# Optimization experiments

Measured on AMD Instinct MI355X. Metric: run time of the kernel, lower is better.

## Reference

```python
import jax, jax.numpy as jnp
import numpy as np

B = 2097152   # number of material points (2**21)
NS = [32, 32] # ICNN hidden widths; output layer is Dense(1)


def setup_inputs() -> dict:
    key = jax.random.key(0)
    ks = jax.random.split(key, 7)
    # Deformation gradients near identity so C = F^T F is invertible.
    F = jnp.eye(3, dtype=jnp.float32)[None, :, :] + 0.05 * jax.random.normal(
        ks[0], (B, 3, 3), dtype=jnp.float32)
    dims = [6] + NS + [1]
    inp = {"F": F}
    for i in range(3):
        # non_neg kernel constraint -> positive weights
        inp[f"W{i}"] = 0.5 * jax.random.uniform(ks[1 + 2 * i], (dims[i], dims[i + 1]),
                                                dtype=jnp.float32)
        inp[f"b{i}"] = 0.1 * jax.random.normal(ks[2 + 2 * i], (dims[i + 1],),
                                               dtype=jnp.float32)
    return inp


def _energy(F, W0, b0, W1, b1, W2, b2):
    """Invariants layer + ICNN -> scalar potential W per sample, shape [B,1]."""
    # C = F^T F, batched 3x3
    C = jnp.einsum('bji,bjk->bik', F, F)
    J = jnp.linalg.det(F)                          # [B]
    cof_C = jnp.linalg.det(C)[:, None, None] * jnp.linalg.inv(C)  # [B,3,3]
    tr = lambda A: jnp.trace(A, axis1=-2, axis2=-1)
    dg = lambda A: jnp.diagonal(A, axis1=-2, axis2=-1)
    I_1 = tr(C)
    I_2 = tr(cof_C)
    # NOTE: TF code uses trace(C ** 2) with ELEMENTWISE square -> sum of squared diagonal
    I_7 = jnp.sum(dg(C) ** 2, axis=-1)
    I_11 = jnp.sum(dg(cof_C) ** 2, axis=-1)
    i = jnp.stack([I_1, I_2, J, -J, I_7, I_11], axis=1)  # [B,6]
    h = jax.nn.softplus(i @ W0 + b0)
    h = jax.nn.softplus(h @ W1 + b1)
    return h @ W2 + b2                              # [B,1]


def reference(F, W0, b0, W1, b1, W2, b2):
    # GradientTape: P = dW/dF (per-sample, since samples are independent)
    Wv, vjp_fn = jax.vjp(lambda f: _energy(f, W0, b0, W1, b1, W2, b2), F)
    P, = vjp_fn(jnp.ones_like(Wv))
    return (P, Wv)
```

## Files before the change

### kernel.cpp

```cpp
#include <hip/hip_runtime.h>
#include <math.h>

typedef __attribute__((ext_vector_type(8)))  short  bf16x8;
typedef __attribute__((ext_vector_type(16))) float  f32x16;

union FragU { unsigned u[4]; bf16x8 s; };

__device__ __forceinline__ float fast_rcp(float x) { return __builtin_amdgcn_rcpf(x); }

__device__ __forceinline__ unsigned cvtpk(float lo, float hi) {
    unsigned r;
    asm("v_cvt_pk_bf16_f32 %0, %1, %2" : "=v"(r) : "v"(lo), "v"(hi));
    return r;
}
__device__ __forceinline__ unsigned pswapu(unsigned x) { return (unsigned)__shfl_xor((int)x, 32, 64); }
__device__ __forceinline__ float    pswapf(float x)    { return __shfl_xor(x, 32, 64); }
__device__ __forceinline__ float bfl(unsigned p) { return __uint_as_float(p << 16); }
__device__ __forceinline__ float bfh(unsigned p) { return __uint_as_float(p & 0xffff0000u); }

__device__ __forceinline__ void sp_sig(float z, float& h, float& s) {
    float az = fabsf(z);
    float e  = __expf(-az);
    float r  = fast_rcp(1.0f + e);
    h = fmaxf(z, 0.0f) + __logf(1.0f + e);
    s = (z >= 0.0f) ? r : (1.0f - r);
}

__device__ __forceinline__ FragU bfrag(bool low, unsigned a0, unsigned a1, unsigned a2, unsigned a3) {
    unsigned s0 = pswapu(a0), s1 = pswapu(a1), s2 = pswapu(a2), s3 = pswapu(a3);
    FragU f;
    f.u[0] = low ? a0 : s2;
    f.u[1] = low ? a1 : s3;
    f.u[2] = low ? s0 : a2;
    f.u[3] = low ? s1 : a3;
    return f;
}

__global__ __launch_bounds__(256) void energy_kernel(
    const float* __restrict__ Fg,
    const float* __restrict__ W0, const float* __restrict__ b0,
    const float* __restrict__ W1, const float* __restrict__ b1,
    const float* __restrict__ W2, const float* __restrict__ b2,
    float* __restrict__ P, float* __restrict__ Wv, int n)
{
    const int  tid  = threadIdx.x;
    const int  lane = tid & 63;
    const int  wid  = tid >> 6;
    const int  col  = lane & 31;
    const int  half = lane >> 5;
    const bool low  = (half == 0);
    const long wave_base = ((long)blockIdx.x * 4 + wid) * 64;
    const long idx  = wave_base + lane;
    const long cidx = (idx < n) ? idx : 0;

    FragU w0t, w1t[2], w1f[2], w0b[2];
    #pragma unroll
    for (int p = 0; p < 4; ++p) {
        const int k0 = half*8 + 2*p, k1 = k0 + 1;
        float lo = (k0 < 6) ? W0[k0*32 + col] : ((k0 == 6) ? b0[col] : 0.f);
        float hi = (k1 < 6) ? W0[k1*32 + col] : ((k1 == 6) ? b0[col] : 0.f);
        w0t.u[p] = cvtpk(lo, hi);
    }
    #pragma unroll
    for (int hf = 0; hf < 2; ++hf) {
        #pragma unroll
        for (int p = 0; p < 4; ++p) {
            const int k0 = hf*16 + half*8 + 2*p, k1 = k0 + 1;
            w1t[hf].u[p] = cvtpk(W1[k0*32 + col], W1[k1*32 + col]);
            w1f[hf].u[p] = cvtpk(W1[col*32 + k0], W1[col*32 + k1]);
            float lo = (col < 6) ? W0[col*32 + k0] : 0.f;
            float hi = (col < 6) ? W0[col*32 + k1] : 0.f;
            w0b[hf].u[p] = cvtpk(lo, hi);
        }
    }
    unsigned b1p[8], w2p[8];
    #pragma unroll
    for (int p = 0; p < 8; ++p) {
        const int r0 = 2*p, r1 = r0 + 1;
        const int R0 = (r0 & 3) + 8*(r0 >> 2) + 4*half;
        const int R1 = (r1 & 3) + 8*(r1 >> 2) + 4*half;
        b1p[p] = cvtpk(b1[R0], b1[R1]);
        w2p[p] = cvtpk(W2[R0], W2[R1]);
    }
    const float b2v = b2[0];

    const float* fp = Fg + cidx * 9;
    float iv0, iv1, iv2, iv4, iv5;
    {
        float f00=fp[0], f01=fp[1], f02=fp[2];
        float f10=fp[3], f11=fp[4], f12=fp[5];
        float f20=fp[6], f21=fp[7], f22=fp[8];

        float c00 = f00*f00 + f10*f10 + f20*f20;
        float c01 = f00*f01 + f10*f11 + f20*f21;
        float c02 = f00*f02 + f10*f12 + f20*f22;
        float c11 = f01*f01 + f11*f11 + f21*f21;
        float c12 = f01*f02 + f11*f12 + f21*f22;
        float c22 = f02*f02 + f12*f12 + f22*f22;

        float A00 = c11*c22 - c12*c12;
        float A01 = c02*c12 - c01*c22;
        float A02 = c01*c12 - c02*c11;
        float A11 = c00*c22 - c02*c02;
        float A12 = c01*c02 - c00*c12;
        float A22 = c00*c11 - c01*c01;

        iv0 = c00 + c11 + c22;
        iv1 = A00 + A11 + A22;
        iv2 = f00*(f11*f22 - f12*f21) - f01*(f10*f22 - f12*f20) + f02*(f10*f21 - f11*f20);
        iv4 = c00*c00 + c11*c11 + c22*c22;
        iv5 = A00*A00 + A11*A11 + A22*A22;
    }

    unsigned V01 = cvtpk(iv0, iv1);
    unsigned V23 = cvtpk(iv2, -iv2);
    unsigned V45 = cvtpk(iv4, iv5);
    const unsigned C67 = cvtpk(1.0f, 0.0f);

    float pt_[2];
    float dk[2][4];

    #pragma unroll
    for (int t = 0; t < 2; ++t) {
        FragU biv;
        if (t == 0) { biv.u[0]=V01;        biv.u[1]=V23;        biv.u[2]=V45;        biv.u[3]=C67; }
        else        { biv.u[0]=pswapu(V01); biv.u[1]=pswapu(V23); biv.u[2]=pswapu(V45); biv.u[3]=C67; }

        f32x16 zz;
        #pragma unroll
        for (int r = 0; r < 16; ++r) zz[r] = 0.f;

        f32x16 z0 = __builtin_amdgcn_mfma_f32_32x32x16_bf16(w0t.s, biv.s, zz, 0, 0, 0);

        unsigned hpk[8], s0p[8];
        #pragma unroll
        for (int p = 0; p < 8; ++p) {
            float ha, sa, hb, sb;
            sp_sig(z0[2*p],   ha, sa);
            sp_sig(z0[2*p+1], hb, sb);
            hpk[p] = cvtpk(ha, hb);
            s0p[p] = cvtpk(sa, sb);
        }
        FragU hb0 = bfrag(low, hpk[0], hpk[1], hpk[2], hpk[3]);
        FragU hb1 = bfrag(low, hpk[4], hpk[5], hpk[6], hpk[7]);

        f32x16 z1;
        #pragma unroll
        for (int p = 0; p < 8; ++p) { z1[2*p] = bfl(b1p[p]); z1[2*p+1] = bfh(b1p[p]); }
        z1 = __builtin_amdgcn_mfma_f32_32x32x16_bf16(w1t[0].s, hb0.s, z1, 0, 0, 0);
        z1 = __builtin_amdgcn_mfma_f32_32x32x16_bf16(w1t[1].s, hb1.s, z1, 0, 0, 0);

        float pt = 0.f;
        unsigned gpk[8];
        #pragma unroll
        for (int p = 0; p < 8; ++p) {
            float h1a, s1a, h1b, s1b;
            sp_sig(z1[2*p],   h1a, s1a);
            sp_sig(z1[2*p+1], h1b, s1b);
            float wa = bfl(w2p[p]), wb = bfh(w2p[p]);
            pt = fmaf(h1a, wa, pt);
            pt = fmaf(h1b, wb, pt);
            gpk[p] = cvtpk(wa * s1a, wb * s1b);
        }
        pt_[t] = pt;
        FragU gb0 = bfrag(low, gpk[0], gpk[1], gpk[2], gpk[3]);
        FragU gb1 = bfrag(low, gpk[4], gpk[5], gpk[6], gpk[7]);

        #pragma unroll
        for (int r = 0; r < 16; ++r) zz[r] = 0.f;
        f32x16 gh = __builtin_amdgcn_mfma_f32_32x32x16_bf16(w1f[0].s, gb0.s, zz, 0, 0, 0);
        gh = __builtin_amdgcn_mfma_f32_32x32x16_bf16(w1f[1].s, gb1.s, gh, 0, 0, 0);

        unsigned qpk[8];
        #pragma unroll
        for (int p = 0; p < 8; ++p)
            qpk[p] = cvtpk(gh[2*p] * bfl(s0p[p]), gh[2*p+1] * bfh(s0p[p]));
        FragU qb0 = bfrag(low, qpk[0], qpk[1], qpk[2], qpk[3]);
        FragU qb1 = bfrag(low, qpk[4], qpk[5], qpk[6], qpk[7]);

        #pragma unroll
        for (int r = 0; r < 16; ++r) zz[r] = 0.f;
        f32x16 da = __builtin_amdgcn_mfma_f32_32x32x16_bf16(w0b[0].s, qb0.s, zz, 0, 0, 0);
        da = __builtin_amdgcn_mfma_f32_32x32x16_bf16(w0b[1].s, qb1.s, da, 0, 0, 0);
        dk[t][0] = da[0]; dk[t][1] = da[1]; dk[t][2] = da[2]; dk[t][3] = da[3];
    }

    float po0 = pswapf(pt_[0]);
    float po1 = pswapf(pt_[1]);
    float wvv = (low ? (pt_[0] + po0) : (pt_[1] + po1)) + b2v;

    float s10 = pswapf(dk[1][0]), s11 = pswapf(dk[1][1]);
    float s12 = pswapf(dk[1][2]), s13 = pswapf(dk[1][3]);
    float s00 = pswapf(dk[0][0]), s01 = pswapf(dk[0][1]);
    float d0  = low ? dk[0][0] : s10;
    float d1  = low ? dk[0][1] : s11;
    float d2r = low ? dk[0][2] : s12;
    float d3r = low ? dk[0][3] : s13;
    float d4  = low ? s00 : dk[1][0];
    float d5  = low ? s01 : dk[1][1];

    float f00=fp[0], f01=fp[1], f02=fp[2];
    float f10=fp[3], f11=fp[4], f12=fp[5];
    float f20=fp[6], f21=fp[7], f22=fp[8];

    float c00 = f00*f00 + f10*f10 + f20*f20;
    float c01 = f00*f01 + f10*f11 + f20*f21;
    float c02 = f00*f02 + f10*f12 + f20*f22;
    float c11 = f01*f01 + f11*f11 + f21*f21;
    float c12 = f01*f02 + f11*f12 + f21*f22;
    float c22 = f02*f02 + f12*f12 + f22*f22;

    float A00 = c11*c22 - c12*c12;
    float A01 = c02*c12 - c01*c22;
    float A02 = c01*c12 - c02*c11;
    float A11 = c00*c22 - c02*c02;
    float A12 = c01*c02 - c00*c12;
    float A22 = c00*c11 - c01*c01;

    float cf00 = f11*f22 - f12*f21;
    float cf01 = f12*f20 - f10*f22;
    float cf02 = f10*f21 - f11*f20;
    float cf10 = f02*f21 - f01*f22;
    float cf11 = f00*f22 - f02*f20;
    float cf12 = f01*f20 - f00*f21;
    float cf20 = f01*f12 - f02*f11;
    float cf21 = f02*f10 - f00*f12;
    float cf22 = f00*f11 - f01*f10;
    float J  = f00*cf00 + f01*cf01 + f02*cf02;
    float I1 = c00 + c11 + c22;
    float I11v = A00*A00 + A11*A11 + A22*A22;

    float inv2 = 2.0f * fast_rcp(J * J);

    float T00 = A00*A00*A00 + A11*A01*A01 + A22*A02*A02;
    float T01 = A00*A00*A01 + A11*A01*A11 + A22*A02*A12;
    float T02 = A00*A00*A02 + A11*A01*A12 + A22*A02*A22;
    float T11 = A00*A01*A01 + A11*A11*A11 + A22*A12*A12;
    float T12 = A00*A01*A02 + A11*A11*A12 + A22*A12*A22;
    float T22 = A00*A02*A02 + A11*A12*A12 + A22*A22*A22;

    float G00 = inv2 * (I11v*A00 - T00);
    float G01 = inv2 * (I11v*A01 - T01);
    float G02 = inv2 * (I11v*A02 - T02);
    float G11e= inv2 * (I11v*A11 - T11);
    float G12 = inv2 * (I11v*A12 - T12);
    float G22 = inv2 * (I11v*A22 - T22);

    float aJ  = d2r - d3r;
    float t1  = 2.0f * d0;
    float t2  = 2.0f * d1;
    float t7  = 4.0f * d4;
    float t11 = 2.0f * d5;

    float m00 = t1 + t2*(I1 - c00) + t7*c00 + t11*G00;
    float m01 =      -t2*c01               + t11*G01;
    float m02 =      -t2*c02               + t11*G02;
    float m11 = t1 + t2*(I1 - c11) + t7*c11 + t11*G11e;
    float m12 =      -t2*c12               + t11*G12;
    float m22 = t1 + t2*(I1 - c22) + t7*c22 + t11*G22;

    if (idx < n) {
        float* p = P + idx * 9;
        p[0] = f00*m00 + f01*m01 + f02*m02 + aJ*cf00;
        p[1] = f00*m01 + f01*m11 + f02*m12 + aJ*cf01;
        p[2] = f00*m02 + f01*m12 + f02*m22 + aJ*cf02;
        p[3] = f10*m00 + f11*m01 + f12*m02 + aJ*cf10;
        p[4] = f10*m01 + f11*m11 + f12*m12 + aJ*cf11;
        p[5] = f10*m02 + f11*m12 + f12*m22 + aJ*cf12;
        p[6] = f20*m00 + f21*m01 + f22*m02 + aJ*cf20;
        p[7] = f20*m01 + f21*m11 + f22*m12 + aJ*cf21;
        p[8] = f20*m02 + f21*m12 + f22*m22 + aJ*cf22;
        Wv[idx] = wvv;
    }
}

extern "C" void kernel_launch(void* const* d_in, const int* in_sizes, int n_in,
                              void* d_out, int out_size, void* d_ws, size_t ws_size,
                              hipStream_t stream) {
    const float* F  = (const float*)d_in[0];
    const float* W0 = (const float*)d_in[1];
    const float* b0 = (const float*)d_in[2];
    const float* W1 = (const float*)d_in[3];
    const float* b1 = (const float*)d_in[4];
    const float* W2 = (const float*)d_in[5];
    const float* b2 = (const float*)d_in[6];
    int n = in_sizes[0] / 9;
    float* out = (float*)d_out;
    float* P  = out;
    float* Wv = out + (size_t)n * 9;

    int block = 256;
    int grid = (n + block - 1) / block;
    hipLaunchKernelGGL(energy_kernel, dim3(grid), dim3(block), 0, stream,
                       F, W0, b0, W1, b1, W2, b2, P, Wv, n);
}
```

Baseline: 135.9 us.

## Prepack MFMA weight fragments and permute K to drop cross-half shuffles

Adds a one-wave pre-kernel that converts the weights to bf16 and stores them in per-lane MFMA fragment order in workspace. The main kernel then fetches them with a few vector loads instead of many scattered scalar loads and conversions per thread. The K index of the W1/W0-back fragments is permuted (rho) so MFMA output registers can feed the next MFMA's B operand directly, which removes the bfrag lane-swap shuffles between layers. This costs an extra kernel launch and a dependency on workspace, and correctness rests on the permutation matching the accumulator layout.

```diff
diff --git a/kernel.cpp b/kernel.cpp
--- a/kernel.cpp
+++ b/kernel.cpp
@@ -4,7 +4,7 @@
 typedef __attribute__((ext_vector_type(8)))  short  bf16x8;
 typedef __attribute__((ext_vector_type(16))) float  f32x16;
 
-union FragU { unsigned u[4]; bf16x8 s; };
+union FragU { unsigned u[4]; bf16x8 s; uint4 q; };
 
 __device__ __forceinline__ float fast_rcp(float x) { return __builtin_amdgcn_rcpf(x); }
 
@@ -17,6 +17,11 @@
 __device__ __forceinline__ float    pswapf(float x)    { return __shfl_xor(x, 32, 64); }
 __device__ __forceinline__ float bfl(unsigned p) { return __uint_as_float(p << 16); }
 __device__ __forceinline__ float bfh(unsigned p) { return __uint_as_float(p & 0xffff0000u); }
+
+__device__ __forceinline__ int rho(int s) {
+    int f = s >> 4, h = (s >> 3) & 1, p = (s >> 1) & 3, j = s & 1;
+    return 16*f + 4*h + 8*(p >> 1) + 2*(p & 1) + j;
+}
 
 __device__ __forceinline__ void sp_sig(float z, float& h, float& s) {
     float az = fabsf(z);
@@ -26,63 +31,86 @@
     s = (z >= 0.0f) ? r : (1.0f - r);
 }
 
-__device__ __forceinline__ FragU bfrag(bool low, unsigned a0, unsigned a1, unsigned a2, unsigned a3) {
-    unsigned s0 = pswapu(a0), s1 = pswapu(a1), s2 = pswapu(a2), s3 = pswapu(a3);
-    FragU f;
-    f.u[0] = low ? a0 : s2;
-    f.u[1] = low ? a1 : s3;
-    f.u[2] = low ? s0 : a2;
-    f.u[3] = low ? s1 : a3;
-    return f;
-}
-
-__global__ __launch_bounds__(256) void energy_kernel(
-    const float* __restrict__ Fg,
+__global__ __launch_bounds__(64) void pack_weights(
     const float* __restrict__ W0, const float* __restrict__ b0,
     const float* __restrict__ W1, const float* __restrict__ b1,
     const float* __restrict__ W2, const float* __restrict__ b2,
+    unsigned* __restrict__ ws)
+{
+    const int lane = threadIdx.x;
+    const int col = lane & 31, half = lane >> 5;
+
+    unsigned v[4];
+    #pragma unroll
+    for (int p = 0; p < 4; ++p) {
+        const int k0 = half*8 + 2*p, k1 = k0 + 1;
+        float lo = (k0 < 6) ? W0[k0*32 + col] : ((k0 == 6) ? b0[col] : 0.f);
+        float hi = (k1 < 6) ? W0[k1*32 + col] : ((k1 == 6) ? b0[col] : 0.f);
+        v[p] = cvtpk(lo, hi);
+    }
+    *(uint4*)(ws + lane*4) = make_uint4(v[0], v[1], v[2], v[3]);
+
+    #pragma unroll
+    for (int hf = 0; hf < 2; ++hf) {
+        unsigned t[4], fq[4], bq[4];
+        #pragma unroll
+        for (int p = 0; p < 4; ++p) {
+            const int s0 = hf*16 + half*8 + 2*p;
+            const int r0 = rho(s0), r1 = r0 + 1;
+            t[p]  = cvtpk(W1[r0*32 + col], W1[r1*32 + col]);
+            fq[p] = cvtpk(W1[col*32 + r0], W1[col*32 + r1]);
+            float lo = (col < 6) ? W0[col*32 + r0] : 0.f;
+            float hi = (col < 6) ? W0[col*32 + r1] : 0.f;
+            bq[p] = cvtpk(lo, hi);
+        }
+        *(uint4*)(ws + 256  + lane*8 + hf*4) = make_uint4(t[0],  t[1],  t[2],  t[3]);
+        *(uint4*)(ws + 768  + lane*8 + hf*4) = make_uint4(fq[0], fq[1], fq[2], fq[3]);
+        *(uint4*)(ws + 1280 + lane*8 + hf*4) = make_uint4(bq[0], bq[1], bq[2], bq[3]);
+    }
+
+    unsigned bp[8], wp[8];
+    #pragma unroll
+    for (int p = 0; p < 8; ++p) {
+        const int r0 = 2*p, r1 = r0 + 1;
+        const int R0 = (r0 & 3) + 8*(r0 >> 2) + 4*half;
+        const int R1 = (r1 & 3) + 8*(r1 >> 2) + 4*half;
+        bp[p] = cvtpk(b1[R0], b1[R1]);
+        wp[p] = cvtpk(W2[R0], W2[R1]);
+    }
+    *(uint4*)(ws + 1792 + lane*8)     = make_uint4(bp[0], bp[1], bp[2], bp[3]);
+    *(uint4*)(ws + 1792 + lane*8 + 4) = make_uint4(bp[4], bp[5], bp[6], bp[7]);
+    *(uint4*)(ws + 2304 + lane*8)     = make_uint4(wp[0], wp[1], wp[2], wp[3]);
+    *(uint4*)(ws + 2304 + lane*8 + 4) = make_uint4(wp[4], wp[5], wp[6], wp[7]);
+    if (lane == 0) ws[2816] = __float_as_uint(b2[0]);
+}
+
+__global__ __launch_bounds__(256) void energy_kernel(
+    const float* __restrict__ Fg,
+    const unsigned* __restrict__ ws,
     float* __restrict__ P, float* __restrict__ Wv, int n)
 {
     const int  tid  = threadIdx.x;
     const int  lane = tid & 63;
     const int  wid  = tid >> 6;
-    const int  col  = lane & 31;
-    const int  half = lane >> 5;
-    const bool low  = (half == 0);
-    const long wave_base = ((long)blockIdx.x * 4 + wid) * 64;
-    const long idx  = wave_base + lane;
+    const bool low  = (lane >> 5) == 0;
+    const long idx  = ((long)blockIdx.x * 4 + wid) * 64 + lane;
     const long cidx = (idx < n) ? idx : 0;
 
     FragU w0t, w1t[2], w1f[2], w0b[2];
-    #pragma unroll
-    for (int p = 0; p < 4; ++p) {
-        const int k0 = half*8 + 2*p, k1 = k0 + 1;
-        float lo = (k0 < 6) ? W0[k0*32 + col] : ((k0 == 6) ? b0[col] : 0.f);
-        float hi = (k1 < 6) ? W0[k1*32 + col] : ((k1 == 6) ? b0[col] : 0.f);
-        w0t.u[p] = cvtpk(lo, hi);
-    }
-    #pragma unroll
-    for (int hf = 0; hf < 2; ++hf) {
-        #pragma unroll
-        for (int p = 0; p < 4; ++p) {
-            const int k0 = hf*16 + half*8 + 2*p, k1 = k0 + 1;
-            w1t[hf].u[p] = cvtpk(W1[k0*32 + col], W1[k1*32 + col]);
-            w1f[hf].u[p] = cvtpk(W1[col*32 + k0], W1[col*32 + k1]);
-            float lo = (col < 6) ? W0[col*32 + k0] : 0.f;
-            float hi = (col < 6) ? W0[col*32 + k1] : 0.f;
-            w0b[hf].u[p] = cvtpk(lo, hi);
-        }
-    }
-    unsigned b1p[8], w2p[8];
-    #pragma unroll
-    for (int p = 0; p < 8; ++p) {
-        const int r0 = 2*p, r1 = r0 + 1;
-        const int R0 = (r0 & 3) + 8*(r0 >> 2) + 4*half;
-        const int R1 = (r1 & 3) + 8*(r1 >> 2) + 4*half;
-        b1p[p] = cvtpk(b1[R0], b1[R1]);
-        w2p[p] = cvtpk(W2[R0], W2[R1]);
-    }
-    const float b2v = b2[0];
+    w0t.q    = *(const uint4*)(ws + lane*4);
+    w1t[0].q = *(const uint4*)(ws + 256  + lane*8);
+    w1t[1].q = *(const uint4*)(ws + 256  + lane*8 + 4);
+    w1f[0].q = *(const uint4*)(ws + 768  + lane*8);
+    w1f[1].q = *(const uint4*)(ws + 768  + lane*8 + 4);
+    w0b[0].q = *(const uint4*)(ws + 1280 + lane*8);
+    w0b[1].q = *(const uint4*)(ws + 1280 + lane*8 + 4);
+    uint4 b1q0 = *(const uint4*)(ws + 1792 + lane*8);
+    uint4 b1q1 = *(const uint4*)(ws + 1792 + lane*8 + 4);
+    uint4 w2q0 = *(const uint4*)(ws + 2304 + lane*8);
+    uint4 w2q1 = *(const uint4*)(ws + 2304 + lane*8 + 4);
+    unsigned b1p[8] = {b1q0.x, b1q0.y, b1q0.z, b1q0.w, b1q1.x, b1q1.y, b1q1.z, b1q1.w};
+    unsigned w2p[8] = {w2q0.x, w2q0.y, w2q0.z, w2q0.w, w2q1.x, w2q1.y, w2q1.z, w2q1.w};
+    const float b2v = __uint_as_float(ws[2816]);
 
     const float* fp = Fg + cidx * 9;
     float iv0, iv1, iv2, iv4, iv5;
@@ -116,6 +144,13 @@
     unsigned V23 = cvtpk(iv2, -iv2);
     unsigned V45 = cvtpk(iv4, iv5);
     const unsigned C67 = cvtpk(1.0f, 0.0f);
+    unsigned S01 = pswapu(V01);
+    unsigned S23 = pswapu(V23);
+    unsigned S45 = pswapu(V45);
+
+    f32x16 zero16;
+    #pragma unroll
+    for (int r = 0; r < 16; ++r) zero16[r] = 0.f;
 
     float pt_[2];
     float dk[2][4];
@@ -123,35 +158,29 @@
     #pragma unroll
     for (int t = 0; t < 2; ++t) {
         FragU biv;
-        if (t == 0) { biv.u[0]=V01;        biv.u[1]=V23;        biv.u[2]=V45;        biv.u[3]=C67; }
-        else        { biv.u[0]=pswapu(V01); biv.u[1]=pswapu(V23); biv.u[2]=pswapu(V45); biv.u[3]=C67; }
-
-        f32x16 zz;
-        #pragma unroll
-        for (int r = 0; r < 16; ++r) zz[r] = 0.f;
-
-        f32x16 z0 = __builtin_amdgcn_mfma_f32_32x32x16_bf16(w0t.s, biv.s, zz, 0, 0, 0);
-
-        unsigned hpk[8], s0p[8];
+        if (t == 0) { biv.u[0]=V01; biv.u[1]=V23; biv.u[2]=V45; biv.u[3]=C67; }
+        else        { biv.u[0]=S01; biv.u[1]=S23; biv.u[2]=S45; biv.u[3]=C67; }
+
+        f32x16 z0 = __builtin_amdgcn_mfma_f32_32x32x16_bf16(w0t.s, biv.s, zero16, 0, 0, 0);
+
+        FragU hbf[2]; unsigned s0p[8];
         #pragma unroll
         for (int p = 0; p < 8; ++p) {
             float ha, sa, hb, sb;
             sp_sig(z0[2*p],   ha, sa);
             sp_sig(z0[2*p+1], hb, sb);
-            hpk[p] = cvtpk(ha, hb);
+            hbf[p >> 2].u[p & 3] = cvtpk(ha, hb);
             s0p[p] = cvtpk(sa, sb);
         }
-        FragU hb0 = bfrag(low, hpk[0], hpk[1], hpk[2], hpk[3]);
-        FragU hb1 = bfrag(low, hpk[4], hpk[5], hpk[6], hpk[7]);
 
         f32x16 z1;
         #pragma unroll
         for (int p = 0; p < 8; ++p) { z1[2*p] = bfl(b1p[p]); z1[2*p+1] = bfh(b1p[p]); }
-        z1 = __builtin_amdgcn_mfma_f32_32x32x16_bf16(w1t[0].s, hb0.s, z1, 0, 0, 0);
-        z1 = __builtin_amdgcn_mfma_f32_32x32x16_bf16(w1t[1].s, hb1.s, z1, 0, 0, 0);
+        z1 = __builtin_amdgcn_mfma_f32_32x32x16_bf16(w1t[0].s, hbf[0].s, z1, 0, 0, 0);
+        z1 = __builtin_amdgcn_mfma_f32_32x32x16_bf16(w1t[1].s, hbf[1].s, z1, 0, 0, 0);
 
         float pt = 0.f;
-        unsigned gpk[8];
+        FragU gbf[2];
         #pragma unroll
         for (int p = 0; p < 8; ++p) {
             float h1a, s1a, h1b, s1b;
@@ -160,28 +189,20 @@
             float wa = bfl(w2p[p]), wb = bfh(w2p[p]);
             pt = fmaf(h1a, wa, pt);
             pt = fmaf(h1b, wb, pt);
-            gpk[p] = cvtpk(wa * s1a, wb * s1b);
+            gbf[p >> 2].u[p & 3] = cvtpk(wa * s1a, wb * s1b);
         }
         pt_[t] = pt;
-        FragU gb0 = bfrag(low, gpk[0], gpk[1], gpk[2], gpk[3]);
-        FragU gb1 = bfrag(low, gpk[4], gpk[5], gpk[6], gpk[7]);
-
-        #pragma unroll
-        for (int r = 0; r < 16; ++r) zz[r] = 0.f;
-        f32x16 gh = __builtin_amdgcn_mfma_f32_32x32x16_bf16(w1f[0].s, gb0.s, zz, 0, 0, 0);
-        gh = __builtin_amdgcn_mfma_f32_32x32x16_bf16(w1f[1].s, gb1.s, gh, 0, 0, 0);
-
-        unsigned qpk[8];
+
+        f32x16 gh = __builtin_amdgcn_mfma_f32_32x32x16_bf16(w1f[0].s, gbf[0].s, zero16, 0, 0, 0);
+        gh = __builtin_amdgcn_mfma_f32_32x32x16_bf16(w1f[1].s, gbf[1].s, gh, 0, 0, 0);
+
+        FragU qbf[2];
         #pragma unroll
         for (int p = 0; p < 8; ++p)
-            qpk[p] = cvtpk(gh[2*p] * bfl(s0p[p]), gh[2*p+1] * bfh(s0p[p]));
-        FragU qb0 = bfrag(low, qpk[0], qpk[1], qpk[2], qpk[3]);
-        FragU qb1 = bfrag(low, qpk[4], qpk[5], qpk[6], qpk[7]);
-
-        #pragma unroll
-        for (int r = 0; r < 16; ++r) zz[r] = 0.f;
-        f32x16 da = __builtin_amdgcn_mfma_f32_32x32x16_bf16(w0b[0].s, qb0.s, zz, 0, 0, 0);
-        da = __builtin_amdgcn_mfma_f32_32x32x16_bf16(w0b[1].s, qb1.s, da, 0, 0, 0);
+            qbf[p >> 2].u[p & 3] = cvtpk(gh[2*p] * bfl(s0p[p]), gh[2*p+1] * bfh(s0p[p]));
+
+        f32x16 da = __builtin_amdgcn_mfma_f32_32x32x16_bf16(w0b[0].s, qbf[0].s, zero16, 0, 0, 0);
+        da = __builtin_amdgcn_mfma_f32_32x32x16_bf16(w0b[1].s, qbf[1].s, da, 0, 0, 0);
         dk[t][0] = da[0]; dk[t][1] = da[1]; dk[t][2] = da[2]; dk[t][3] = da[3];
     }
 
@@ -288,9 +309,13 @@
     float* out = (float*)d_out;
     float* P  = out;
     float* Wv = out + (size_t)n * 9;
+    unsigned* ws = (unsigned*)d_ws;
+
+    hipLaunchKernelGGL(pack_weights, dim3(1), dim3(64), 0, stream,
+                       W0, b0, W1, b1, W2, b2, ws);
 
     int block = 256;
     int grid = (n + block - 1) / block;
     hipLaunchKernelGGL(energy_kernel, dim3(grid), dim3(block), 0, stream,
-                       F, W0, b0, W1, b1, W2, b2, P, Wv, n);
-}
+                       F, ws, P, Wv, n);
+}
```

After: 118.6 us. -12.7%, faster.
